# Kernel optimization log

Measured on AMD Instinct MI355X. Metric: run time of the kernel, lower is better.

## Reference

```python
import jax, jax.numpy as jnp
import numpy as np

D = 1024  # input_size == context_size
B, SQ, SKV = 4, 2048, 2048


def setup_inputs() -> dict:
    key = jax.random.key(0)
    ks = jax.random.split(key, 8)
    s = 1.0 / np.sqrt(D)
    return {
        "x": jax.random.normal(ks[0], (B, SQ, D), jnp.float32),
        "context": jax.random.normal(ks[1], (B, SKV, D), jnp.float32),
        "Wq": jax.random.uniform(ks[2], (D, D), jnp.float32, -s, s),
        "bq": jnp.zeros((D,), jnp.float32),
        "Wk": jax.random.uniform(ks[3], (D, D), jnp.float32, -s, s),
        "bk": jnp.zeros((D,), jnp.float32),
        "Wv": jax.random.uniform(ks[4], (D, D), jnp.float32, -s, s),
        "bv": jnp.zeros((D,), jnp.float32),
    }


def reference(x, context, Wq, bq, Wk, bk, Wv, bv):
    # Linear layers (torch nn.Linear: y = x @ W^T + b; here W stored as [in, out])
    Q = x @ Wq + bq                  # [B, SQ, D]
    K = context @ Wk + bk            # [B, SKV, D]
    V = context @ Wv + bv            # [B, SKV, D]
    scale = 1.0 / np.sqrt(D).astype(np.float32)
    scores = jnp.einsum("bqd,bkd->bqk", Q, K) * scale  # [B, SQ, SKV]
    attn = jax.nn.softmax(scores, axis=-1)
    out = jnp.einsum("bqk,bkd->bqd", attn, V)          # [B, SQ, D]
    return out
```

## Files before the change

### kernel.cpp

```cpp
#include <hip/hip_runtime.h>
#include <cstdint>
#include <cstddef>

typedef __attribute__((ext_vector_type(8))) short short8;
typedef __attribute__((ext_vector_type(4))) float floatx4;

__device__ __forceinline__ unsigned short f2bf(float f) {
    union { float f; unsigned int u; } v; v.f = f;
    unsigned int r = v.u + 0x7fffu + ((v.u >> 16) & 1u);
    return (unsigned short)(r >> 16);
}
__device__ __forceinline__ float bf2f(unsigned short h) {
    union { unsigned int u; float f; } v; v.u = ((unsigned int)h) << 16;
    return v.f;
}

__device__ __forceinline__ void glds16(const void* g, void* l) {
    __builtin_amdgcn_global_load_lds(
        (const __attribute__((address_space(1))) void*)g,
        (__attribute__((address_space(3))) void*)l, 16, 0, 0);
}

__device__ __forceinline__ void gemm_core(
    const unsigned short* __restrict__ Ab, int ldA,
    const unsigned short* __restrict__ Bb, int ldB,
    int K,
    unsigned short* __restrict__ As, unsigned short* __restrict__ Bs,
    floatx4 (&acc)[4][4])
{
    const int tid = threadIdx.x;
    const int wave = tid >> 6, lane = tid & 63;

    const unsigned short* gA[4];
    const unsigned short* gB[4];
#pragma unroll
    for (int i = 0; i < 4; ++i) {
        const int c = i * 256 + tid;
        const int row = c >> 3;
        const int l = (c & 7) ^ (row & 7);
        gA[i] = Ab + (size_t)row * ldA + l * 8;
        gB[i] = Bb + (size_t)row * ldB + l * 8;
    }
    const int arow = (wave >> 1) * 64 + (lane & 15);
    const int brow = (wave & 1) * 64 + (lane & 15);
    const int p0 = (lane >> 4) ^ (lane & 7);
    const unsigned short* pa0 = As + arow * 64 + p0 * 8;
    const unsigned short* pb0 = Bs + brow * 64 + p0 * 8;
    const unsigned short* pa1 = As + arow * 64 + (p0 ^ 4) * 8;
    const unsigned short* pb1 = Bs + brow * 64 + (p0 ^ 4) * 8;

    for (int k0 = 0; k0 < K; k0 += 64) {
#pragma unroll
        for (int i = 0; i < 4; ++i)
            glds16(gA[i] + k0, As + (size_t)(i * 256 + wave * 64) * 8);
#pragma unroll
        for (int i = 0; i < 4; ++i)
            glds16(gB[i] + k0, Bs + (size_t)(i * 256 + wave * 64) * 8);
        __syncthreads();
        short8 a0[4], b0[4], a1[4], b1[4];
#pragma unroll
        for (int mt = 0; mt < 4; ++mt) a0[mt] = *(const short8*)(pa0 + mt * 16 * 64);
#pragma unroll
        for (int nt = 0; nt < 4; ++nt) b0[nt] = *(const short8*)(pb0 + nt * 16 * 64);
#pragma unroll
        for (int mt = 0; mt < 4; ++mt)
#pragma unroll
            for (int nt = 0; nt < 4; ++nt)
                acc[mt][nt] = __builtin_amdgcn_mfma_f32_16x16x32_bf16(a0[mt], b0[nt], acc[mt][nt], 0, 0, 0);
#pragma unroll
        for (int mt = 0; mt < 4; ++mt) a1[mt] = *(const short8*)(pa1 + mt * 16 * 64);
#pragma unroll
        for (int nt = 0; nt < 4; ++nt) b1[nt] = *(const short8*)(pb1 + nt * 16 * 64);
#pragma unroll
        for (int mt = 0; mt < 4; ++mt)
#pragma unroll
            for (int nt = 0; nt < 4; ++nt)
                acc[mt][nt] = __builtin_amdgcn_mfma_f32_16x16x32_bf16(a1[mt], b1[nt], acc[mt][nt], 0, 0, 0);
        __syncthreads();
    }
}

__global__ __launch_bounds__(256) void cvt2_kernel(
    const float* __restrict__ x, const float* __restrict__ ctx,
    unsigned short* __restrict__ xb, unsigned short* __restrict__ cb) {
    int i = blockIdx.x * blockDim.x + threadIdx.x;
    const float* in; unsigned short* out; int j;
    if (i < 2097152) { in = x; out = xb; j = i; }
    else { in = ctx; out = cb; j = i - 2097152; }
    float4 v = reinterpret_cast<const float4*>(in)[j];
    ushort4 o;
    o.x = f2bf(v.x); o.y = f2bf(v.y); o.z = f2bf(v.z); o.w = f2bf(v.w);
    reinterpret_cast<ushort4*>(out)[j] = o;
}

__global__ __launch_bounds__(256) void wtr_kernel(
    const float* __restrict__ Wq, const float* __restrict__ Wk, const float* __restrict__ Wv,
    unsigned short* __restrict__ Wt0, unsigned short* __restrict__ WtKV) {
    __shared__ float tile[32][33];
    const int z = blockIdx.z;
    const float* in = (z == 0) ? Wq : (z == 1) ? Wk : Wv;
    unsigned short* out = (z == 0) ? Wt0 : (z == 1) ? WtKV : (WtKV + 1024 * 1024);
    int c0 = blockIdx.x * 32, r0 = blockIdx.y * 32;
    int tx = threadIdx.x, ty = threadIdx.y;
#pragma unroll
    for (int j = 0; j < 4; ++j)
        tile[ty + j * 8][tx] = in[(size_t)(r0 + ty + j * 8) * 1024 + c0 + tx];
    __syncthreads();
#pragma unroll
    for (int j = 0; j < 4; ++j)
        out[(size_t)(c0 + ty + j * 8) * 1024 + r0 + tx] = f2bf(tile[tx][ty + j * 8]);
}

__global__ __launch_bounds__(256) void qkv_kernel(
    const unsigned short* __restrict__ xb, const unsigned short* __restrict__ cb,
    const unsigned short* __restrict__ WtQ, const unsigned short* __restrict__ WtKV,
    const float* __restrict__ bq, const float* __restrict__ bk, const float* __restrict__ bv,
    unsigned short* __restrict__ Qb, unsigned short* __restrict__ Kb,
    unsigned short* __restrict__ Vt) {
    __shared__ unsigned short As[128 * 64];
    __shared__ unsigned short Bs[128 * 64];
    const int vb = blockIdx.x;
    const bool isQ = vb < 512;
    int by, bxcol;
    const unsigned short *A, *B;
    if (isQ) {
        by = vb >> 3; const int bx = vb & 7; bxcol = bx * 128;
        A = xb + (size_t)by * 128 * 1024;
        B = WtQ + (size_t)bx * 128 * 1024;
    } else {
        const int v = vb - 512;
        by = v >> 4; const int bx = v & 15; bxcol = bx * 128;
        A = cb + (size_t)by * 128 * 1024;
        B = WtKV + (size_t)bx * 128 * 1024;
    }
    floatx4 acc[4][4];
#pragma unroll
    for (int i = 0; i < 4; ++i)
#pragma unroll
        for (int j = 0; j < 4; ++j) acc[i][j] = (floatx4){0.f, 0.f, 0.f, 0.f};

    gemm_core(A, 1024, B, 1024, 1024, As, Bs, acc);

    const int wave = threadIdx.x >> 6, lane = threadIdx.x & 63;
    const int cm = by * 128 + (wave >> 1) * 64 + (lane >> 4) * 4;
    const int cn = bxcol + (wave & 1) * 64 + (lane & 15);
    if (isQ || bxcol < 1024) {
        unsigned short* O = isQ ? Qb : Kb;
        const float* bias = isQ ? bq : bk;
#pragma unroll
        for (int nt = 0; nt < 4; ++nt) {
            const int col = cn + nt * 16;
            const float bvv = bias[col];
#pragma unroll
            for (int mt = 0; mt < 4; ++mt)
#pragma unroll
                for (int r = 0; r < 4; ++r)
                    O[(size_t)(cm + mt * 16 + r) * 1024 + col] = f2bf(acc[mt][nt][r] + bvv);
        }
    } else {
#pragma unroll
        for (int nt = 0; nt < 4; ++nt) {
            const int colv = cn + nt * 16 - 1024;
            const float bvv = bv[colv];
#pragma unroll
            for (int mt = 0; mt < 4; ++mt) {
                const int rowg = cm + mt * 16;
                const int b = rowg >> 11, q = rowg & 2047;
                ushort4 u;
                u.x = f2bf(acc[mt][nt][0] + bvv);
                u.y = f2bf(acc[mt][nt][1] + bvv);
                u.z = f2bf(acc[mt][nt][2] + bvv);
                u.w = f2bf(acc[mt][nt][3] + bvv);
                *reinterpret_cast<ushort4*>(Vt + (size_t)b * 2097152 + (size_t)colv * 2048 + q) = u;
            }
        }
    }
}

__global__ __launch_bounds__(256) void qkt_kernel(
    const unsigned short* __restrict__ Qb, const unsigned short* __restrict__ Kb,
    unsigned short* __restrict__ Sb) {
    __shared__ unsigned short As[128 * 64];
    __shared__ unsigned short Bs[128 * 64];
    const int z = blockIdx.z;
    const unsigned short* A = Qb + (size_t)z * 2048 * 1024 + (size_t)blockIdx.y * 128 * 1024;
    const unsigned short* B = Kb + (size_t)z * 2048 * 1024 + (size_t)blockIdx.x * 128 * 1024;
    floatx4 acc[4][4];
#pragma unroll
    for (int i = 0; i < 4; ++i)
#pragma unroll
        for (int j = 0; j < 4; ++j) acc[i][j] = (floatx4){0.f, 0.f, 0.f, 0.f};

    gemm_core(A, 1024, B, 1024, 1024, As, Bs, acc);

    const int wave = threadIdx.x >> 6, lane = threadIdx.x & 63;
    unsigned short* C = Sb + (size_t)z * 2048 * 2048;
    const int cm = blockIdx.y * 128 + (wave >> 1) * 64 + (lane >> 4) * 4;
    const int cn = blockIdx.x * 128 + (wave & 1) * 64 + (lane & 15);
#pragma unroll
    for (int nt = 0; nt < 4; ++nt)
#pragma unroll
        for (int mt = 0; mt < 4; ++mt)
#pragma unroll
            for (int r = 0; r < 4; ++r)
                C[(size_t)(cm + mt * 16 + r) * 2048 + cn + nt * 16] = f2bf(acc[mt][nt][r]);
}

__global__ __launch_bounds__(256) void pv_kernel(
    const unsigned short* __restrict__ Sb, const unsigned short* __restrict__ Vt,
    float* __restrict__ out) {
    __shared__ unsigned short As[128 * 64];
    __shared__ unsigned short Bs[128 * 64];
    const int z = blockIdx.z;
    const unsigned short* A = Sb + (size_t)z * 2048 * 2048 + (size_t)blockIdx.y * 128 * 2048;
    const unsigned short* B = Vt + (size_t)z * 1024 * 2048 + (size_t)blockIdx.x * 128 * 2048;
    floatx4 acc[4][4];
#pragma unroll
    for (int i = 0; i < 4; ++i)
#pragma unroll
        for (int j = 0; j < 4; ++j) acc[i][j] = (floatx4){0.f, 0.f, 0.f, 0.f};

    gemm_core(A, 2048, B, 2048, 2048, As, Bs, acc);

    const int wave = threadIdx.x >> 6, lane = threadIdx.x & 63;
    float* C = out + (size_t)z * 2048 * 1024;
    const int cm = blockIdx.y * 128 + (wave >> 1) * 64 + (lane >> 4) * 4;
    const int cn = blockIdx.x * 128 + (wave & 1) * 64 + (lane & 15);
#pragma unroll
    for (int nt = 0; nt < 4; ++nt)
#pragma unroll
        for (int mt = 0; mt < 4; ++mt)
#pragma unroll
            for (int r = 0; r < 4; ++r)
                C[(size_t)(cm + mt * 16 + r) * 1024 + cn + nt * 16] = acc[mt][nt][r];
}

__global__ __launch_bounds__(256) void softmax_kernel(unsigned short* __restrict__ S, float scale) {
    unsigned short* row = S + (size_t)blockIdx.x * 2048;
    const int t = threadIdx.x;
    ushort4 u0 = reinterpret_cast<const ushort4*>(row)[t * 2];
    ushort4 u1 = reinterpret_cast<const ushort4*>(row)[t * 2 + 1];
    float v[8];
    v[0] = bf2f(u0.x) * scale; v[1] = bf2f(u0.y) * scale;
    v[2] = bf2f(u0.z) * scale; v[3] = bf2f(u0.w) * scale;
    v[4] = bf2f(u1.x) * scale; v[5] = bf2f(u1.y) * scale;
    v[6] = bf2f(u1.z) * scale; v[7] = bf2f(u1.w) * scale;

    float lm = v[0];
#pragma unroll
    for (int j = 1; j < 8; ++j) lm = fmaxf(lm, v[j]);
#pragma unroll
    for (int o = 32; o > 0; o >>= 1) lm = fmaxf(lm, __shfl_xor(lm, o));

    __shared__ float red[8];
    const int wv = t >> 6;
    if ((t & 63) == 0) red[wv] = lm;
    __syncthreads();
    const float rm = fmaxf(fmaxf(red[0], red[1]), fmaxf(red[2], red[3]));

    float s = 0.f;
#pragma unroll
    for (int j = 0; j < 8; ++j) { v[j] = __expf(v[j] - rm); s += v[j]; }
#pragma unroll
    for (int o = 32; o > 0; o >>= 1) s += __shfl_xor(s, o);
    if ((t & 63) == 0) red[4 + wv] = s;
    __syncthreads();
    const float inv = 1.f / (red[4] + red[5] + red[6] + red[7]);

    ushort4 o0, o1;
    o0.x = f2bf(v[0] * inv); o0.y = f2bf(v[1] * inv);
    o0.z = f2bf(v[2] * inv); o0.w = f2bf(v[3] * inv);
    o1.x = f2bf(v[4] * inv); o1.y = f2bf(v[5] * inv);
    o1.z = f2bf(v[6] * inv); o1.w = f2bf(v[7] * inv);
    reinterpret_cast<ushort4*>(row)[t * 2] = o0;
    reinterpret_cast<ushort4*>(row)[t * 2 + 1] = o1;
}

extern "C" void kernel_launch(void* const* d_in, const int* in_sizes, int n_in,
                              void* d_out, int out_size, void* d_ws, size_t ws_size,
                              hipStream_t stream) {
    const float* x   = (const float*)d_in[0];
    const float* ctx = (const float*)d_in[1];
    const float* Wq  = (const float*)d_in[2];
    const float* bq  = (const float*)d_in[3];
    const float* Wk  = (const float*)d_in[4];
    const float* bk  = (const float*)d_in[5];
    const float* Wv  = (const float*)d_in[6];
    const float* bv  = (const float*)d_in[7];
    float* out = (float*)d_out;

    const size_t MB = 1024 * 1024;
    char* ws = (char*)d_ws;
    unsigned short* xb   = (unsigned short*)(ws + 0 * MB);
    unsigned short* cb   = (unsigned short*)(ws + 16 * MB);
    unsigned short* Qb   = (unsigned short*)(ws + 32 * MB);
    unsigned short* Kb   = (unsigned short*)(ws + 48 * MB);
    unsigned short* Vt   = (unsigned short*)(ws + 64 * MB);
    unsigned short* Wt0  = (unsigned short*)(ws + 80 * MB);
    unsigned short* WtKV = (unsigned short*)(ws + 82 * MB);
    unsigned short* Sb   = (unsigned short*)(ws + 86 * MB);

    cvt2_kernel<<<16384, 256, 0, stream>>>(x, ctx, xb, cb);
    wtr_kernel<<<dim3(32, 32, 3), dim3(32, 8), 0, stream>>>(Wq, Wk, Wv, Wt0, WtKV);
    qkv_kernel<<<1536, 256, 0, stream>>>(xb, cb, Wt0, WtKV, bq, bk, bv, Qb, Kb, Vt);
    qkt_kernel<<<dim3(16, 16, 4), 256, 0, stream>>>(Qb, Kb, Sb);
    softmax_kernel<<<8192, 256, 0, stream>>>(Sb, 0.03125f);
    pv_kernel<<<dim3(8, 16, 4), 256, 0, stream>>>(Sb, Vt, out);
}
```

Baseline: 294.7 us.

## Switch GEMMs to 32x32x16 MFMA, merge prep kernels, fold scale into QK^T

The shared GEMM core now uses 32x32x16 bf16 MFMA with 2x2 floatx16 accumulators per wave instead of 4x4 16x16x32 tiles, and every epilogue is remapped to the new output layout. The conversion and weight-transpose kernels are merged into one launch, and the softmax scale is applied in the QK^T epilogue so softmax no longer multiplies. Launch bounds with a minimum of 3 blocks per CU are added to the GEMM kernels. The larger MFMA shape is meant to cut LDS reads and instruction count per FLOP, but the register hint could cause spills, and scaling before bf16 rounding slightly changes numerics.

```diff
diff --git a/kernel.cpp b/kernel.cpp
--- a/kernel.cpp
+++ b/kernel.cpp
@@ -4,6 +4,7 @@
 
 typedef __attribute__((ext_vector_type(8))) short short8;
 typedef __attribute__((ext_vector_type(4))) float floatx4;
+typedef __attribute__((ext_vector_type(16))) float floatx16;
 
 __device__ __forceinline__ unsigned short f2bf(float f) {
     union { float f; unsigned int u; } v; v.f = f;
@@ -26,7 +27,7 @@
     const unsigned short* __restrict__ Bb, int ldB,
     int K,
     unsigned short* __restrict__ As, unsigned short* __restrict__ Bs,
-    floatx4 (&acc)[4][4])
+    floatx16 (&acc)[2][2])
 {
     const int tid = threadIdx.x;
     const int wave = tid >> 6, lane = tid & 63;
@@ -41,13 +42,12 @@
         gA[i] = Ab + (size_t)row * ldA + l * 8;
         gB[i] = Bb + (size_t)row * ldB + l * 8;
     }
-    const int arow = (wave >> 1) * 64 + (lane & 15);
-    const int brow = (wave & 1) * 64 + (lane & 15);
-    const int p0 = (lane >> 4) ^ (lane & 7);
-    const unsigned short* pa0 = As + arow * 64 + p0 * 8;
-    const unsigned short* pb0 = Bs + brow * 64 + p0 * 8;
-    const unsigned short* pa1 = As + arow * 64 + (p0 ^ 4) * 8;
-    const unsigned short* pb1 = Bs + brow * 64 + (p0 ^ 4) * 8;
+    const int arow = (wave >> 1) * 64 + (lane & 31);
+    const int brow = (wave & 1) * 64 + (lane & 31);
+    const int kg = lane >> 5;
+    const int sw = lane & 7;
+    const unsigned short* pa = As + arow * 64;
+    const unsigned short* pb = Bs + brow * 64;
 
     for (int k0 = 0; k0 < K; k0 += 64) {
 #pragma unroll
@@ -57,61 +57,58 @@
         for (int i = 0; i < 4; ++i)
             glds16(gB[i] + k0, Bs + (size_t)(i * 256 + wave * 64) * 8);
         __syncthreads();
-        short8 a0[4], b0[4], a1[4], b1[4];
-#pragma unroll
-        for (int mt = 0; mt < 4; ++mt) a0[mt] = *(const short8*)(pa0 + mt * 16 * 64);
-#pragma unroll
-        for (int nt = 0; nt < 4; ++nt) b0[nt] = *(const short8*)(pb0 + nt * 16 * 64);
-#pragma unroll
-        for (int mt = 0; mt < 4; ++mt)
-#pragma unroll
-            for (int nt = 0; nt < 4; ++nt)
-                acc[mt][nt] = __builtin_amdgcn_mfma_f32_16x16x32_bf16(a0[mt], b0[nt], acc[mt][nt], 0, 0, 0);
-#pragma unroll
-        for (int mt = 0; mt < 4; ++mt) a1[mt] = *(const short8*)(pa1 + mt * 16 * 64);
-#pragma unroll
-        for (int nt = 0; nt < 4; ++nt) b1[nt] = *(const short8*)(pb1 + nt * 16 * 64);
-#pragma unroll
-        for (int mt = 0; mt < 4; ++mt)
-#pragma unroll
-            for (int nt = 0; nt < 4; ++nt)
-                acc[mt][nt] = __builtin_amdgcn_mfma_f32_16x16x32_bf16(a1[mt], b1[nt], acc[mt][nt], 0, 0, 0);
+#pragma unroll
+        for (int s = 0; s < 4; ++s) {
+            const int off = ((2 * s + kg) ^ sw) * 8;
+            short8 a0 = *(const short8*)(pa + off);
+            short8 a1 = *(const short8*)(pa + 32 * 64 + off);
+            short8 b0 = *(const short8*)(pb + off);
+            short8 b1 = *(const short8*)(pb + 32 * 64 + off);
+            acc[0][0] = __builtin_amdgcn_mfma_f32_32x32x16_bf16(a0, b0, acc[0][0], 0, 0, 0);
+            acc[0][1] = __builtin_amdgcn_mfma_f32_32x32x16_bf16(a0, b1, acc[0][1], 0, 0, 0);
+            acc[1][0] = __builtin_amdgcn_mfma_f32_32x32x16_bf16(a1, b0, acc[1][0], 0, 0, 0);
+            acc[1][1] = __builtin_amdgcn_mfma_f32_32x32x16_bf16(a1, b1, acc[1][1], 0, 0, 0);
+        }
         __syncthreads();
     }
 }
 
-__global__ __launch_bounds__(256) void cvt2_kernel(
+#define EPI_ROW(r, kg) (((r) & 3) + 8 * ((r) >> 2) + 4 * (kg))
+
+__global__ __launch_bounds__(256) void prep_kernel(
     const float* __restrict__ x, const float* __restrict__ ctx,
-    unsigned short* __restrict__ xb, unsigned short* __restrict__ cb) {
-    int i = blockIdx.x * blockDim.x + threadIdx.x;
-    const float* in; unsigned short* out; int j;
-    if (i < 2097152) { in = x; out = xb; j = i; }
-    else { in = ctx; out = cb; j = i - 2097152; }
-    float4 v = reinterpret_cast<const float4*>(in)[j];
-    ushort4 o;
-    o.x = f2bf(v.x); o.y = f2bf(v.y); o.z = f2bf(v.z); o.w = f2bf(v.w);
-    reinterpret_cast<ushort4*>(out)[j] = o;
-}
-
-__global__ __launch_bounds__(256) void wtr_kernel(
     const float* __restrict__ Wq, const float* __restrict__ Wk, const float* __restrict__ Wv,
+    unsigned short* __restrict__ xb, unsigned short* __restrict__ cb,
     unsigned short* __restrict__ Wt0, unsigned short* __restrict__ WtKV) {
-    __shared__ float tile[32][33];
-    const int z = blockIdx.z;
-    const float* in = (z == 0) ? Wq : (z == 1) ? Wk : Wv;
-    unsigned short* out = (z == 0) ? Wt0 : (z == 1) ? WtKV : (WtKV + 1024 * 1024);
-    int c0 = blockIdx.x * 32, r0 = blockIdx.y * 32;
-    int tx = threadIdx.x, ty = threadIdx.y;
-#pragma unroll
-    for (int j = 0; j < 4; ++j)
-        tile[ty + j * 8][tx] = in[(size_t)(r0 + ty + j * 8) * 1024 + c0 + tx];
-    __syncthreads();
-#pragma unroll
-    for (int j = 0; j < 4; ++j)
-        out[(size_t)(c0 + ty + j * 8) * 1024 + r0 + tx] = f2bf(tile[tx][ty + j * 8]);
-}
-
-__global__ __launch_bounds__(256) void qkv_kernel(
+    const int b = blockIdx.x;
+    if (b < 16384) {
+        int i = b * 256 + threadIdx.x;
+        const float* in; unsigned short* out; int j;
+        if (i < 2097152) { in = x; out = xb; j = i; }
+        else { in = ctx; out = cb; j = i - 2097152; }
+        float4 v = reinterpret_cast<const float4*>(in)[j];
+        ushort4 o;
+        o.x = f2bf(v.x); o.y = f2bf(v.y); o.z = f2bf(v.z); o.w = f2bf(v.w);
+        reinterpret_cast<ushort4*>(out)[j] = o;
+    } else {
+        __shared__ float tile[32][33];
+        const int z = b - 16384;
+        const int w = z >> 10, t = z & 1023;
+        const float* in = (w == 0) ? Wq : (w == 1) ? Wk : Wv;
+        unsigned short* out = (w == 0) ? Wt0 : (w == 1) ? WtKV : (WtKV + 1024 * 1024);
+        const int c0 = (t & 31) * 32, r0 = (t >> 5) * 32;
+        const int tx = threadIdx.x & 31, ty = threadIdx.x >> 5;
+#pragma unroll
+        for (int j = 0; j < 4; ++j)
+            tile[ty + j * 8][tx] = in[(size_t)(r0 + ty + j * 8) * 1024 + c0 + tx];
+        __syncthreads();
+#pragma unroll
+        for (int j = 0; j < 4; ++j)
+            out[(size_t)(c0 + ty + j * 8) * 1024 + r0 + tx] = f2bf(tile[tx][ty + j * 8]);
+    }
+}
+
+__global__ __launch_bounds__(256, 3) void qkv_kernel(
     const unsigned short* __restrict__ xb, const unsigned short* __restrict__ cb,
     const unsigned short* __restrict__ WtQ, const unsigned short* __restrict__ WtKV,
     const float* __restrict__ bq, const float* __restrict__ bk, const float* __restrict__ bv,
@@ -133,51 +130,60 @@
         A = cb + (size_t)by * 128 * 1024;
         B = WtKV + (size_t)bx * 128 * 1024;
     }
-    floatx4 acc[4][4];
-#pragma unroll
-    for (int i = 0; i < 4; ++i)
-#pragma unroll
-        for (int j = 0; j < 4; ++j) acc[i][j] = (floatx4){0.f, 0.f, 0.f, 0.f};
+    floatx16 acc[2][2];
+#pragma unroll
+    for (int i = 0; i < 2; ++i)
+#pragma unroll
+        for (int j = 0; j < 2; ++j)
+#pragma unroll
+            for (int r = 0; r < 16; ++r) acc[i][j][r] = 0.f;
 
     gemm_core(A, 1024, B, 1024, 1024, As, Bs, acc);
 
     const int wave = threadIdx.x >> 6, lane = threadIdx.x & 63;
-    const int cm = by * 128 + (wave >> 1) * 64 + (lane >> 4) * 4;
-    const int cn = bxcol + (wave & 1) * 64 + (lane & 15);
+    const int kg = lane >> 5;
+    const int cm = by * 128 + (wave >> 1) * 64;
+    const int cn = bxcol + (wave & 1) * 64 + (lane & 31);
     if (isQ || bxcol < 1024) {
         unsigned short* O = isQ ? Qb : Kb;
         const float* bias = isQ ? bq : bk;
 #pragma unroll
-        for (int nt = 0; nt < 4; ++nt) {
-            const int col = cn + nt * 16;
+        for (int nt = 0; nt < 2; ++nt) {
+            const int col = cn + nt * 32;
             const float bvv = bias[col];
 #pragma unroll
-            for (int mt = 0; mt < 4; ++mt)
-#pragma unroll
-                for (int r = 0; r < 4; ++r)
-                    O[(size_t)(cm + mt * 16 + r) * 1024 + col] = f2bf(acc[mt][nt][r] + bvv);
+            for (int mt = 0; mt < 2; ++mt)
+#pragma unroll
+                for (int r = 0; r < 16; ++r) {
+                    const int row = cm + mt * 32 + EPI_ROW(r, kg);
+                    O[(size_t)row * 1024 + col] = f2bf(acc[mt][nt][r] + bvv);
+                }
         }
     } else {
 #pragma unroll
-        for (int nt = 0; nt < 4; ++nt) {
-            const int colv = cn + nt * 16 - 1024;
+        for (int nt = 0; nt < 2; ++nt) {
+            const int colv = cn + nt * 32 - 1024;
             const float bvv = bv[colv];
 #pragma unroll
-            for (int mt = 0; mt < 4; ++mt) {
-                const int rowg = cm + mt * 16;
-                const int b = rowg >> 11, q = rowg & 2047;
-                ushort4 u;
-                u.x = f2bf(acc[mt][nt][0] + bvv);
-                u.y = f2bf(acc[mt][nt][1] + bvv);
-                u.z = f2bf(acc[mt][nt][2] + bvv);
-                u.w = f2bf(acc[mt][nt][3] + bvv);
-                *reinterpret_cast<ushort4*>(Vt + (size_t)b * 2097152 + (size_t)colv * 2048 + q) = u;
+            for (int mt = 0; mt < 2; ++mt) {
+                const int rowg = cm + mt * 32 + 4 * kg;
+                const int b = rowg >> 11, qb = rowg & 2047;
+#pragma unroll
+                for (int g = 0; g < 4; ++g) {
+                    const int q = qb + 8 * g;
+                    ushort4 u;
+                    u.x = f2bf(acc[mt][nt][g * 4 + 0] + bvv);
+                    u.y = f2bf(acc[mt][nt][g * 4 + 1] + bvv);
+                    u.z = f2bf(acc[mt][nt][g * 4 + 2] + bvv);
+                    u.w = f2bf(acc[mt][nt][g * 4 + 3] + bvv);
+                    *reinterpret_cast<ushort4*>(Vt + (size_t)b * 2097152 + (size_t)colv * 2048 + q) = u;
+                }
             }
         }
     }
 }
 
-__global__ __launch_bounds__(256) void qkt_kernel(
+__global__ __launch_bounds__(256, 3) void qkt_kernel(
     const unsigned short* __restrict__ Qb, const unsigned short* __restrict__ Kb,
     unsigned short* __restrict__ Sb) {
     __shared__ unsigned short As[128 * 64];
@@ -185,28 +191,33 @@
     const int z = blockIdx.z;
     const unsigned short* A = Qb + (size_t)z * 2048 * 1024 + (size_t)blockIdx.y * 128 * 1024;
     const unsigned short* B = Kb + (size_t)z * 2048 * 1024 + (size_t)blockIdx.x * 128 * 1024;
-    floatx4 acc[4][4];
-#pragma unroll
-    for (int i = 0; i < 4; ++i)
-#pragma unroll
-        for (int j = 0; j < 4; ++j) acc[i][j] = (floatx4){0.f, 0.f, 0.f, 0.f};
+    floatx16 acc[2][2];
+#pragma unroll
+    for (int i = 0; i < 2; ++i)
+#pragma unroll
+        for (int j = 0; j < 2; ++j)
+#pragma unroll
+            for (int r = 0; r < 16; ++r) acc[i][j][r] = 0.f;
 
     gemm_core(A, 1024, B, 1024, 1024, As, Bs, acc);
 
     const int wave = threadIdx.x >> 6, lane = threadIdx.x & 63;
+    const int kg = lane >> 5;
     unsigned short* C = Sb + (size_t)z * 2048 * 2048;
-    const int cm = blockIdx.y * 128 + (wave >> 1) * 64 + (lane >> 4) * 4;
-    const int cn = blockIdx.x * 128 + (wave & 1) * 64 + (lane & 15);
-#pragma unroll
-    for (int nt = 0; nt < 4; ++nt)
-#pragma unroll
-        for (int mt = 0; mt < 4; ++mt)
-#pragma unroll
-            for (int r = 0; r < 4; ++r)
-                C[(size_t)(cm + mt * 16 + r) * 2048 + cn + nt * 16] = f2bf(acc[mt][nt][r]);
-}
-
-__global__ __launch_bounds__(256) void pv_kernel(
+    const int cm = blockIdx.y * 128 + (wave >> 1) * 64;
+    const int cn = blockIdx.x * 128 + (wave & 1) * 64 + (lane & 31);
+#pragma unroll
+    for (int nt = 0; nt < 2; ++nt)
+#pragma unroll
+        for (int mt = 0; mt < 2; ++mt)
+#pragma unroll
+            for (int r = 0; r < 16; ++r) {
+                const int row = cm + mt * 32 + EPI_ROW(r, kg);
+                C[(size_t)row * 2048 + cn + nt * 32] = f2bf(acc[mt][nt][r] * 0.03125f);
+            }
+}
+
+__global__ __launch_bounds__(256, 3) void pv_kernel(
     const unsigned short* __restrict__ Sb, const unsigned short* __restrict__ Vt,
     float* __restrict__ out) {
     __shared__ unsigned short As[128 * 64];
@@ -214,37 +225,40 @@
     const int z = blockIdx.z;
     const unsigned short* A = Sb + (size_t)z * 2048 * 2048 + (size_t)blockIdx.y * 128 * 2048;
     const unsigned short* B = Vt + (size_t)z * 1024 * 2048 + (size_t)blockIdx.x * 128 * 2048;
-    floatx4 acc[4][4];
-#pragma unroll
-    for (int i = 0; i < 4; ++i)
-#pragma unroll
-        for (int j = 0; j < 4; ++j) acc[i][j] = (floatx4){0.f, 0.f, 0.f, 0.f};
+    floatx16 acc[2][2];
+#pragma unroll
+    for (int i = 0; i < 2; ++i)
+#pragma unroll
+        for (int j = 0; j < 2; ++j)
+#pragma unroll
+            for (int r = 0; r < 16; ++r) acc[i][j][r] = 0.f;
 
     gemm_core(A, 2048, B, 2048, 2048, As, Bs, acc);
 
     const int wave = threadIdx.x >> 6, lane = threadIdx.x & 63;
+    const int kg = lane >> 5;
     float* C = out + (size_t)z * 2048 * 1024;
-    const int cm = blockIdx.y * 128 + (wave >> 1) * 64 + (lane >> 4) * 4;
-    const int cn = blockIdx.x * 128 + (wave & 1) * 64 + (lane & 15);
-#pragma unroll
-    for (int nt = 0; nt < 4; ++nt)
-#pragma unroll
-        for (int mt = 0; mt < 4; ++mt)
-#pragma unroll
-            for (int r = 0; r < 4; ++r)
-                C[(size_t)(cm + mt * 16 + r) * 1024 + cn + nt * 16] = acc[mt][nt][r];
-}
-
-__global__ __launch_bounds__(256) void softmax_kernel(unsigned short* __restrict__ S, float scale) {
+    const int cm = blockIdx.y * 128 + (wave >> 1) * 64;
+    const int cn = blockIdx.x * 128 + (wave & 1) * 64 + (lane & 31);
+#pragma unroll
+    for (int nt = 0; nt < 2; ++nt)
+#pragma unroll
+        for (int mt = 0; mt < 2; ++mt)
+#pragma unroll
+            for (int r = 0; r < 16; ++r) {
+                const int row = cm + mt * 32 + EPI_ROW(r, kg);
+                C[(size_t)row * 1024 + cn + nt * 32] = acc[mt][nt][r];
+            }
+}
+
+__global__ __launch_bounds__(256) void softmax_kernel(unsigned short* __restrict__ S) {
     unsigned short* row = S + (size_t)blockIdx.x * 2048;
     const int t = threadIdx.x;
     ushort4 u0 = reinterpret_cast<const ushort4*>(row)[t * 2];
     ushort4 u1 = reinterpret_cast<const ushort4*>(row)[t * 2 + 1];
     float v[8];
-    v[0] = bf2f(u0.x) * scale; v[1] = bf2f(u0.y) * scale;
-    v[2] = bf2f(u0.z) * scale; v[3] = bf2f(u0.w) * scale;
-    v[4] = bf2f(u1.x) * scale; v[5] = bf2f(u1.y) * scale;
-    v[6] = bf2f(u1.z) * scale; v[7] = bf2f(u1.w) * scale;
+    v[0] = bf2f(u0.x); v[1] = bf2f(u0.y); v[2] = bf2f(u0.z); v[3] = bf2f(u0.w);
+    v[4] = bf2f(u1.x); v[5] = bf2f(u1.y); v[6] = bf2f(u1.z); v[7] = bf2f(u1.w);
 
     float lm = v[0];
 #pragma unroll
@@ -300,10 +314,9 @@
     unsigned short* WtKV = (unsigned short*)(ws + 82 * MB);
     unsigned short* Sb   = (unsigned short*)(ws + 86 * MB);
 
-    cvt2_kernel<<<16384, 256, 0, stream>>>(x, ctx, xb, cb);
-    wtr_kernel<<<dim3(32, 32, 3), dim3(32, 8), 0, stream>>>(Wq, Wk, Wv, Wt0, WtKV);
+    prep_kernel<<<16384 + 3072, 256, 0, stream>>>(x, ctx, Wq, Wk, Wv, xb, cb, Wt0, WtKV);
     qkv_kernel<<<1536, 256, 0, stream>>>(xb, cb, Wt0, WtKV, bq, bk, bv, Qb, Kb, Vt);
     qkt_kernel<<<dim3(16, 16, 4), 256, 0, stream>>>(Qb, Kb, Sb);
-    softmax_kernel<<<8192, 256, 0, stream>>>(Sb, 0.03125f);
+    softmax_kernel<<<8192, 256, 0, stream>>>(Sb);
     pv_kernel<<<dim3(8, 16, 4), 256, 0, stream>>>(Sb, Vt, out);
 }
```

Result: slower. 301.6 us (+2.3%).
